# Kernel optimization log

Hardware: AMD Instinct MI355X
Metric: run time of the kernel (lower is better)

Reference implementation:

```python
import jax, jax.numpy as jnp
import numpy as np

B, S, E, H, I = 32, 257, 1024, 16, 4096
D = E // H  # head_dim = 64
EPS = 1e-5


def setup_inputs() -> dict:
    key = jax.random.key(0)
    ks = jax.random.split(key, 12)
    std = 0.02
    inp = {
        'hidden_states': jax.random.normal(ks[0], (B, S, E), jnp.float32),
        'attention_mask': jnp.zeros((B, 1, S, S), jnp.float32),
        'causal_attention_mask': jnp.zeros((B, 1, S, S), jnp.float32),
        'ln1_w': jnp.ones((E,), jnp.float32),
        'ln1_b': jnp.zeros((E,), jnp.float32),
        'q_w': jax.random.normal(ks[1], (E, E), jnp.float32) * std,
        'q_b': jnp.zeros((E,), jnp.float32),
        'k_w': jax.random.normal(ks[2], (E, E), jnp.float32) * std,
        'k_b': jnp.zeros((E,), jnp.float32),
        'v_w': jax.random.normal(ks[3], (E, E), jnp.float32) * std,
        'v_b': jnp.zeros((E,), jnp.float32),
        'o_w': jax.random.normal(ks[4], (E, E), jnp.float32) * std,
        'o_b': jnp.zeros((E,), jnp.float32),
        'ln2_w': jnp.ones((E,), jnp.float32),
        'ln2_b': jnp.zeros((E,), jnp.float32),
        'fc1_w': jax.random.normal(ks[5], (I, E), jnp.float32) * std,
        'fc1_b': jnp.zeros((I,), jnp.float32),
        'fc2_w': jax.random.normal(ks[6], (E, I), jnp.float32) * std,
        'fc2_b': jnp.zeros((E,), jnp.float32),
    }
    return inp


def _layernorm(x, w, b):
    mu = jnp.mean(x, axis=-1, keepdims=True)
    var = jnp.mean(jnp.square(x - mu), axis=-1, keepdims=True)
    return (x - mu) * jax.lax.rsqrt(var + EPS) * w + b


def _gelu_tanh(x):
    # 0.5*x*(1+tanh(sqrt(2/pi)*(x+0.044715*x^3)))
    c = np.sqrt(2.0 / np.pi).astype(np.float32)
    return 0.5 * x * (1.0 + jnp.tanh(c * (x + 0.044715 * x * x * x)))


def reference(hidden_states, attention_mask, causal_attention_mask,
              ln1_w, ln1_b, q_w, q_b, k_w, k_b, v_w, v_b, o_w, o_b,
              ln2_w, ln2_b, fc1_w, fc1_b, fc2_w, fc2_b):
    scale = D ** -0.5
    residual = hidden_states
    x = _layernorm(hidden_states, ln1_w, ln1_b)

    # projections (torch Linear: x @ W.T + b), q pre-scaled as in source
    q = (x @ q_w.T + q_b) * scale
    k = x @ k_w.T + k_b
    v = x @ v_w.T + v_b

    # [B, H, S, D]
    q = q.reshape(B, S, H, D).transpose(0, 2, 1, 3)
    k = k.reshape(B, S, H, D).transpose(0, 2, 1, 3)
    v = v.reshape(B, S, H, D).transpose(0, 2, 1, 3)

    scores = jnp.einsum('bhqd,bhkd->bhqk', q, k)  # [B,H,S,S]
    scores = scores + causal_attention_mask + attention_mask
    probs = jax.nn.softmax(scores, axis=-1)
    ctx = jnp.einsum('bhqk,bhkd->bhqd', probs, v)
    ctx = ctx.transpose(0, 2, 1, 3).reshape(B, S, E)
    attn_out = ctx @ o_w.T + o_b

    h = residual + attn_out
    residual = h
    x = _layernorm(h, ln2_w, ln2_b)
    x = _gelu_tanh(x @ fc1_w.T + fc1_b)
    x = x @ fc2_w.T + fc2_b
    return residual + x
```

## Files before the change

kernel.cpp:

```cpp
#include <hip/hip_runtime.h>

typedef unsigned short u16;
typedef unsigned int   u32;
typedef short s16x8 __attribute__((ext_vector_type(8)));
typedef float f32x4 __attribute__((ext_vector_type(4)));

#define MFMA16(A,B,C) __builtin_amdgcn_mfma_f32_16x16x32_bf16((A),(B),(C),0,0,0)
#define BAR()  asm volatile("s_barrier" ::: "memory")
#define LGKM0  asm volatile("s_waitcnt lgkmcnt(0)" ::: "memory")
#define VMC2   asm volatile("s_waitcnt vmcnt(2)" ::: "memory")
#define VMC0   asm volatile("s_waitcnt vmcnt(0)" ::: "memory")

#define B_   32
#define S_   257
#define E_   1024
#define H_   16
#define D_   64
#define I_   4096
#define M_   (B_*S_)

__device__ __forceinline__ u16 f2bf(float f) {
    u32 u = __float_as_uint(f);
    u32 r = u + 0x7fffu + ((u >> 16) & 1u);
    return (u16)(r >> 16);
}
__device__ __forceinline__ float bf2f(u16 b) {
    return __uint_as_float(((u32)b) << 16);
}

__device__ __forceinline__ void gload16(const void* g, void* l) {
    __builtin_amdgcn_global_load_lds(
        (const __attribute__((address_space(1))) u32*)g,
        (__attribute__((address_space(3))) u32*)l, 16, 0, 0);
}

__global__ __launch_bounds__(256)
void convert_w_kernel(const float* __restrict__ qw, const float* __restrict__ kw,
                      const float* __restrict__ vw, const float* __restrict__ ow,
                      const float* __restrict__ f1, const float* __restrict__ f2,
                      u16* __restrict__ dst)
{
    const int total4 = (12 * 1048576) / 4;
    for (int i = blockIdx.x * 256 + threadIdx.x; i < total4; i += gridDim.x * 256) {
        int e = i * 4;
        int seg = e >> 20;
        const float* srcp; int off;
        if (seg < 4)      { srcp = (seg == 0 ? qw : seg == 1 ? kw : seg == 2 ? vw : ow); off = e & 1048575; }
        else if (seg < 8) { srcp = f1; off = e - 4 * 1048576; }
        else              { srcp = f2; off = e - 8 * 1048576; }
        float4 v = *(const float4*)(srcp + off);
        ushort4 o;
        o.x = f2bf(v.x); o.y = f2bf(v.y); o.z = f2bf(v.z); o.w = f2bf(v.w);
        *(ushort4*)(dst + e) = o;
    }
}

__global__ __launch_bounds__(256)
void mask_combine_kernel(const float* __restrict__ am, const float* __restrict__ cm,
                         u16* __restrict__ msum)
{
    const int total = B_ * S_ * 272;
    for (int i = blockIdx.x * 256 + threadIdx.x; i < total; i += gridDim.x * 256) {
        int skv = i % 272;
        int rem = i / 272;
        int sq  = rem % S_;
        int b   = rem / S_;
        float v;
        if (skv < S_) {
            size_t o = ((size_t)b * S_ + sq) * S_ + skv;
            v = am[o] + cm[o];
        } else v = -1e30f;
        msum[i] = f2bf(v);
    }
}

__global__ __launch_bounds__(256)
void ln_kernel(const float* __restrict__ src, const float* __restrict__ gam,
               const float* __restrict__ bet, u16* __restrict__ dst)
{
    int row = blockIdx.x;
    const float4* p = (const float4*)(src + (size_t)row * E_);
    float4 x = p[threadIdx.x];
    float s  = x.x + x.y + x.z + x.w;
    float s2 = x.x * x.x + x.y * x.y + x.z * x.z + x.w * x.w;
#pragma unroll
    for (int xm = 1; xm < 64; xm <<= 1) {
        s  += __shfl_xor(s,  xm, 64);
        s2 += __shfl_xor(s2, xm, 64);
    }
    __shared__ float red[8];
    int wv = threadIdx.x >> 6;
    if ((threadIdx.x & 63) == 0) { red[wv] = s; red[4 + wv] = s2; }
    __syncthreads();
    s  = red[0] + red[1] + red[2] + red[3];
    s2 = red[4] + red[5] + red[6] + red[7];
    float mu  = s * (1.0f / 1024.0f);
    float var = s2 * (1.0f / 1024.0f) - mu * mu;
    float rs  = rsqrtf(var + 1e-5f);
    float4 g  = ((const float4*)gam)[threadIdx.x];
    float4 be = ((const float4*)bet)[threadIdx.x];
    ushort4 o;
    o.x = f2bf((x.x - mu) * rs * g.x + be.x);
    o.y = f2bf((x.y - mu) * rs * g.y + be.y);
    o.z = f2bf((x.z - mu) * rs * g.z + be.z);
    o.w = f2bf((x.w - mu) * rs * g.w + be.w);
    ((ushort4*)dst)[(size_t)row * 256 + threadIdx.x] = o;
}

template<int MODE>
__global__ __launch_bounds__(512, 2)
void gemm8(const u16* __restrict__ A,
           const u16* __restrict__ Bq, const u16* __restrict__ Bk, const u16* __restrict__ Bv,
           const float* __restrict__ biasq, const float* __restrict__ biask, const float* __restrict__ biasvv,
           const float* __restrict__ res, float* __restrict__ outF, float* __restrict__ outF1,
           u16* __restrict__ outBq, u16* __restrict__ outBk, u16* __restrict__ outBv,
           int M, int N, int Ks, int klen)
{
    __shared__ u16 lds[2][4][8192];
    const int tid = threadIdx.x, lane = tid & 63, w = tid >> 6;
    const int lr = lane & 15, lg = lane >> 4;
    const int wm = w >> 2, wn = w & 3;

    const u16* Bm = Bq; const float* bias = biasq; u16* outB = outBq;
    float scl = 1.0f; int nt = blockIdx.x; int k0 = 0; float* outP = outF;
    if (MODE == 0) {
        int mat = nt >> 2; nt &= 3;
        if (mat == 1)      { Bm = Bk; bias = biask; outB = outBk; }
        else if (mat == 2) { Bm = Bv; bias = biasvv; outB = outBv; }
        if (mat == 0) scl = 0.125f;
    } else if (MODE == 3) {
        int kz = nt & 1; nt >>= 1;
        k0 = kz * klen;
        if (kz) outP = outF1;
    }
    const int m0 = blockIdx.y * 256, n0 = nt * 256;
    const int NT = klen >> 6, NI = klen >> 7;
    const int tb = k0 >> 6;

    {
    }
    const int p    = w * 1024 + lane * 16;
    const int lby  = p ^ (((p >> 7) & 7) << 4);
    const int srow = lby >> 7;
    const int scol = (lby & 127) >> 1;

    auto STAGE = [&](int buf, int half, const u16* src, int grow0, int rowmax, int t) {
#pragma unroll
        for (int s = 0; s < 2; ++s) {
            int gr = grow0 + s * 64 + srow; if (gr > rowmax) gr = rowmax;
            gload16(src + (size_t)gr * Ks + ((tb + t) << 6) + scol,
                    (char*)&lds[buf][half][0] + s * 8192 + w * 1024);
        }
    };
    auto LDA = [&](int buf, int mh, int mf, int kh) -> s16x8 {
        const char* b = (const char*)&lds[buf][wm][0];
        int inrow = mh * 64 + mf * 16 + lr;
        return *(const s16x8*)(b + inrow * 128 + ((kh * 64 + lg * 16) ^ ((lr & 7) << 4)));
    };
    auto LDB = [&](int buf, int nh, int nf, int kh) -> s16x8 {
        const char* b = (const char*)&lds[buf][2 + (wn >> 1)][0];
        int inrow = (wn & 1) * 64 + nh * 32 + nf * 16 + lr;
        return *(const s16x8*)(b + inrow * 128 + ((kh * 64 + lg * 16) ^ ((lr & 7) << 4)));
    };

    f32x4 acc[8][4];
#pragma unroll
    for (int i = 0; i < 8; ++i)
#pragma unroll
        for (int j = 0; j < 4; ++j) { f32x4 z = {0.f, 0.f, 0.f, 0.f}; acc[i][j] = z; }

    s16x8 a[4][2], b[2][2][2];
    auto MFQ = [&](int mh, int nh) {
        __builtin_amdgcn_s_setprio(1);
#pragma unroll
        for (int mf = 0; mf < 4; ++mf)
#pragma unroll
            for (int nf = 0; nf < 2; ++nf)
#pragma unroll
                for (int kh = 0; kh < 2; ++kh)
                    acc[mh * 4 + mf][nh * 2 + nf] =
                        MFMA16(a[mf][kh], b[nh][nf][kh], acc[mh * 4 + mf][nh * 2 + nf]);
        __builtin_amdgcn_s_setprio(0);
    };

    STAGE(0, 0, A,  m0,       M - 1, 0);
    STAGE(0, 1, A,  m0 + 128, M - 1, 0);
    STAGE(0, 2, Bm, n0,       N - 1, 0);
    STAGE(0, 3, Bm, n0 + 128, N - 1, 0);
    STAGE(1, 0, A,  m0,       M - 1, 1);
    VMC2;
    BAR();

    for (int i = 0; i < NI; ++i) {
        const int t1 = 2 * i + 1, t2 = 2 * i + 2, t3 = 2 * i + 3;
        const bool more = (i + 1 < NI);
#pragma unroll
        for (int mf = 0; mf < 4; ++mf)
#pragma unroll
            for (int kh = 0; kh < 2; ++kh) a[mf][kh] = LDA(0, 0, mf, kh);
#pragma unroll
        for (int nf = 0; nf < 2; ++nf)
#pragma unroll
            for (int kh = 0; kh < 2; ++kh) b[0][nf][kh] = LDB(0, 0, nf, kh);
        STAGE(1, 1, A, m0 + 128, M - 1, t1);
        BAR(); LGKM0;
        MFQ(0, 0);
        BAR();
#pragma unroll
        for (int nf = 0; nf < 2; ++nf)
#pragma unroll
            for (int kh = 0; kh < 2; ++kh) b[1][nf][kh] = LDB(0, 1, nf, kh);
        STAGE(1, 2, Bm, n0, N - 1, t1);
        BAR(); LGKM0;
        MFQ(0, 1);
        BAR();
#pragma unroll
        for (int mf = 0; mf < 4; ++mf)
#pragma unroll
            for (int kh = 0; kh < 2; ++kh) a[mf][kh] = LDA(0, 1, mf, kh);
        STAGE(1, 3, Bm, n0 + 128, N - 1, t1);
        BAR(); LGKM0;
        MFQ(1, 1);
        BAR();
        if (more) STAGE(0, 0, A, m0, M - 1, t2);
        MFQ(1, 0);
        if (more) { VMC2; } else { VMC0; }
        BAR();
#pragma unroll
        for (int mf = 0; mf < 4; ++mf)
#pragma unroll
            for (int kh = 0; kh < 2; ++kh) a[mf][kh] = LDA(1, 0, mf, kh);
#pragma unroll
        for (int nf = 0; nf < 2; ++nf)
#pragma unroll
            for (int kh = 0; kh < 2; ++kh) b[0][nf][kh] = LDB(1, 0, nf, kh);
        if (more) STAGE(0, 2, Bm, n0, N - 1, t2);
        BAR(); LGKM0;
        MFQ(0, 0);
        BAR();
#pragma unroll
        for (int nf = 0; nf < 2; ++nf)
#pragma unroll
            for (int kh = 0; kh < 2; ++kh) b[1][nf][kh] = LDB(1, 1, nf, kh);
        if (more) STAGE(0, 3, Bm, n0 + 128, N - 1, t2);
        BAR(); LGKM0;
        MFQ(0, 1);
        BAR();
#pragma unroll
        for (int mf = 0; mf < 4; ++mf)
#pragma unroll
            for (int kh = 0; kh < 2; ++kh) a[mf][kh] = LDA(1, 1, mf, kh);
        if (more) STAGE(0, 1, A, m0 + 128, M - 1, t2);
        BAR(); LGKM0;
        MFQ(1, 1);
        BAR();
        if (more) STAGE(1, 0, A, m0, M - 1, t3);
        MFQ(1, 0);
        if (more) VMC2;
        BAR();
    }

    float biasv[4];
    if (MODE != 3) {
#pragma unroll
        for (int an = 0; an < 4; ++an)
            biasv[an] = bias[n0 + wn * 64 + (an >> 1) * 32 + (an & 1) * 16 + lr];
    }
#pragma unroll
    for (int am = 0; am < 8; ++am) {
#pragma unroll
        for (int r = 0; r < 4; ++r) {
            int row = m0 + wm * 128 + (am >> 2) * 64 + (am & 3) * 16 + lg * 4 + r;
            if (row >= M) continue;
            if (MODE == 0) {
                int bb = row / S_;
                int ss = row - bb * S_;
#pragma unroll
                for (int an = 0; an < 4; ++an) {
                    int col = n0 + wn * 64 + (an >> 1) * 32 + (an & 1) * 16 + lr;
                    int hh = col >> 6, dd = col & 63;
                    float v = (acc[am][an][r] + biasv[an]) * scl;
                    outB[(((size_t)bb * H_ + hh) * S_ + ss) * D_ + dd] = f2bf(v);
                }
            } else if (MODE == 1) {
                size_t base = (size_t)row * N;
#pragma unroll
                for (int an = 0; an < 4; ++an) {
                    int col = n0 + wn * 64 + (an >> 1) * 32 + (an & 1) * 16 + lr;
                    outF[base + col] = acc[am][an][r] + biasv[an] + res[base + col];
                }
            } else if (MODE == 2) {
                size_t base = (size_t)row * N;
#pragma unroll
                for (int an = 0; an < 4; ++an) {
                    int col = n0 + wn * 64 + (an >> 1) * 32 + (an & 1) * 16 + lr;
                    float x = acc[am][an][r] + biasv[an];
                    float u = 0.7978845608028654f * (x + 0.044715f * x * x * x);
                    float t = tanhf(u);
                    outB[base + col] = f2bf(0.5f * x * (1.0f + t));
                }
            } else {
                size_t base = (size_t)row * N;
#pragma unroll
                for (int an = 0; an < 4; ++an) {
                    int col = n0 + wn * 64 + (an >> 1) * 32 + (an & 1) * 16 + lr;
                    outP[base + col] = acc[am][an][r];
                }
            }
        }
    }
}

__global__ __launch_bounds__(256)
void fc2_reduce(const float* __restrict__ P0, const float* __restrict__ P1,
                const float* __restrict__ res, const float* __restrict__ bias,
                float* __restrict__ out)
{
    const int n4 = (M_ * E_) / 4;
    for (int i = blockIdx.x * 256 + threadIdx.x; i < n4; i += gridDim.x * 256) {
        float4 x0 = ((const float4*)P0)[i];
        float4 x1 = ((const float4*)P1)[i];
        float4 rr = ((const float4*)res)[i];
        float4 bb = ((const float4*)bias)[i & 255];
        float4 o;
        o.x = x0.x + x1.x + rr.x + bb.x;
        o.y = x0.y + x1.y + rr.y + bb.y;
        o.z = x0.z + x1.z + rr.z + bb.z;
        o.w = x0.w + x1.w + rr.w + bb.w;
        ((float4*)out)[i] = o;
    }
}

__global__ __launch_bounds__(256)
void attn_kernel(const u16* __restrict__ qg_, const u16* __restrict__ kg_,
                 const u16* __restrict__ vg_, const u16* __restrict__ msum,
                 u16* __restrict__ ctx)
{
    __shared__ u16 Ks[272 * 72];
    __shared__ u16 Vt[64 * 296];
    __shared__ u16 Ps[4][16 * 32];
    const int bh = blockIdx.x;
    const int b = bh >> 4, hh = bh & 15;
    const u16* kg = kg_ + (size_t)bh * (S_ * D_);
    const u16* vg = vg_ + (size_t)bh * (S_ * D_);
    const u16* qg = qg_ + (size_t)bh * (S_ * D_);
    const int tid = threadIdx.x, lane = tid & 63, wv = tid >> 6;

    for (int c = tid; c < (S_ * D_) / 8; c += 256) {
        int s = c >> 3, d8 = (c & 7) << 3;
        s16x8 val = *(const s16x8*)(kg + s * 64 + d8);
        *(s16x8*)&Ks[s * 72 + d8] = val;
    }
    for (int idx = tid; idx < 15 * 64; idx += 256) {
        int rr = 257 + (idx >> 6), cc = idx & 63;
        Ks[rr * 72 + cc] = 0;
    }
    for (int c = tid; c < (S_ * D_) / 8; c += 256) {
        int s = c >> 3, d8 = (c & 7) << 3;
        s16x8 val = *(const s16x8*)(vg + s * 64 + d8);
#pragma unroll
        for (int j = 0; j < 8; ++j) Vt[(d8 + j) * 296 + s] = (u16)val[j];
    }
    for (int idx = tid; idx < 64 * 39; idx += 256) {
        int dd = idx / 39, cc = 257 + idx % 39;
        Vt[dd * 296 + cc] = 0;
    }
    __syncthreads();

    const int lr = lane & 15, lg = lane >> 4;
    for (int qb = wv; qb < 17; qb += 4) {
        const int q0 = qb * 16;
        int qrow = q0 + lr; if (qrow > S_ - 1) qrow = S_ - 1;
        s16x8 aq0 = *(const s16x8*)(qg + qrow * 64 + lg * 8);
        s16x8 aq1 = *(const s16x8*)(qg + qrow * 64 + 32 + lg * 8);

        f32x4 sc[17];
#pragma unroll
        for (int t = 0; t < 17; ++t) { f32x4 z = {0.f, 0.f, 0.f, 0.f}; sc[t] = z; }
#pragma unroll
        for (int t = 0; t < 17; ++t) {
            s16x8 b0 = *(const s16x8*)&Ks[(t * 16 + lr) * 72 + lg * 8];
            s16x8 b1 = *(const s16x8*)&Ks[(t * 16 + lr) * 72 + 32 + lg * 8];
            sc[t] = MFMA16(aq0, b0, sc[t]);
            sc[t] = MFMA16(aq1, b1, sc[t]);
        }
        float mx[4] = {-3e38f, -3e38f, -3e38f, -3e38f};
#pragma unroll
        for (int r = 0; r < 4; ++r) {
            int sq = q0 + lg * 4 + r; if (sq > S_ - 1) sq = S_ - 1;
            const u16* mrow = msum + ((size_t)b * S_ + sq) * 272;
#pragma unroll
            for (int t = 0; t < 17; ++t) {
                sc[t][r] += bf2f(mrow[t * 16 + lr]);
                mx[r] = fmaxf(mx[r], sc[t][r]);
            }
        }
#pragma unroll
        for (int r = 0; r < 4; ++r) {
#pragma unroll
            for (int xm = 1; xm <= 8; xm <<= 1)
                mx[r] = fmaxf(mx[r], __shfl_xor(mx[r], xm, 64));
        }
        float sum[4] = {0.f, 0.f, 0.f, 0.f};
#pragma unroll
        for (int t = 0; t < 17; ++t)
#pragma unroll
            for (int r = 0; r < 4; ++r) {
                float e = __expf(sc[t][r] - mx[r]);
                sc[t][r] = e; sum[r] += e;
            }
#pragma unroll
        for (int r = 0; r < 4; ++r) {
#pragma unroll
            for (int xm = 1; xm <= 8; xm <<= 1)
                sum[r] += __shfl_xor(sum[r], xm, 64);
        }

        f32x4 ac[4];
#pragma unroll
        for (int nt = 0; nt < 4; ++nt) { f32x4 z = {0.f, 0.f, 0.f, 0.f}; ac[nt] = z; }
        u16* myP = &Ps[wv][0];
#pragma unroll
        for (int kc = 0; kc < 9; ++kc) {
#pragma unroll
            for (int tt = 0; tt < 2; ++tt) {
                const int t = kc * 2 + tt;
#pragma unroll
                for (int r = 0; r < 4; ++r) {
                    float pv = (t < 17) ? sc[(t < 17) ? t : 0][r] : 0.f;
                    myP[(lg * 4 + r) * 32 + tt * 16 + lr] = f2bf(pv);
                }
            }
            s16x8 pa = *(const s16x8*)&myP[lr * 32 + lg * 8];
#pragma unroll
            for (int nt = 0; nt < 4; ++nt) {
                s16x8 bv = *(const s16x8*)&Vt[(nt * 16 + lr) * 296 + kc * 32 + lg * 8];
                ac[nt] = MFMA16(pa, bv, ac[nt]);
            }
        }
#pragma unroll
        for (int r = 0; r < 4; ++r) {
            int sq = q0 + lg * 4 + r;
            if (sq < S_) {
                float rd = 1.0f / sum[r];
                size_t base = (((size_t)b * S_ + sq) * H_ + hh) * D_;
#pragma unroll
                for (int nt = 0; nt < 4; ++nt)
                    ctx[base + nt * 16 + lr] = f2bf(ac[nt][r] * rd);
            }
        }
    }
}

extern "C" void kernel_launch(void* const* d_in, const int* in_sizes, int n_in,
                              void* d_out, int out_size, void* d_ws, size_t ws_size,
                              hipStream_t stream)
{
    const float* hid   = (const float*)d_in[0];
    const float* am    = (const float*)d_in[1];
    const float* cm    = (const float*)d_in[2];
    const float* ln1w  = (const float*)d_in[3];
    const float* ln1b  = (const float*)d_in[4];
    const float* qw    = (const float*)d_in[5];
    const float* qbias = (const float*)d_in[6];
    const float* kw    = (const float*)d_in[7];
    const float* kbias = (const float*)d_in[8];
    const float* vw    = (const float*)d_in[9];
    const float* vbias = (const float*)d_in[10];
    const float* ow    = (const float*)d_in[11];
    const float* obias = (const float*)d_in[12];
    const float* ln2w  = (const float*)d_in[13];
    const float* ln2b  = (const float*)d_in[14];
    const float* f1w   = (const float*)d_in[15];
    const float* f1b   = (const float*)d_in[16];
    const float* f2w   = (const float*)d_in[17];
    const float* f2b   = (const float*)d_in[18];
    float* out = (float*)d_out;

    const size_t ME = (size_t)M_ * E_;
    u16* Wq   = (u16*)d_ws;
    u16* Wk   = Wq + 1048576;
    u16* Wv   = Wk + 1048576;
    u16* Wo   = Wv + 1048576;
    u16* Wf1  = Wo + 1048576;
    u16* Wf2  = Wf1 + 4 * 1048576;
    u16* xln  = Wf2 + 4 * 1048576;
    u16* qb_  = xln + ME;
    u16* kb_  = qb_ + ME;
    u16* vb_  = kb_ + ME;
    u16* ctx  = vb_ + ME;
    float* hbuf = (float*)(ctx + ME);
    u16* msum = (u16*)(hbuf + ME);
    u16* act  = qb_;
    u16* x2   = xln;
    float* P0 = (float*)(msum + (size_t)B_ * S_ * 272);
    float* P1 = P0 + ME;
    const size_t need = (size_t)((char*)(P1 + ME) - (char*)d_ws);
    const bool split = ws_size >= need;

    convert_w_kernel<<<3072, 256, 0, stream>>>(qw, kw, vw, ow, f1w, f2w, Wq);
    mask_combine_kernel<<<8736, 256, 0, stream>>>(am, cm, msum);
    ln_kernel<<<M_, 256, 0, stream>>>(hid, ln1w, ln1b, xln);
    gemm8<0><<<dim3(12, 33), 512, 0, stream>>>(xln, Wq, Wk, Wv, qbias, kbias, vbias,
                                               nullptr, nullptr, nullptr, qb_, kb_, vb_,
                                               M_, 1024, 1024, 1024);
    attn_kernel<<<512, 256, 0, stream>>>(qb_, kb_, vb_, msum, ctx);
    gemm8<1><<<dim3(4, 33), 512, 0, stream>>>(ctx, Wo, nullptr, nullptr, obias, nullptr, nullptr,
                                              hid, hbuf, nullptr, nullptr, nullptr, nullptr,
                                              M_, 1024, 1024, 1024);
    ln_kernel<<<M_, 256, 0, stream>>>(hbuf, ln2w, ln2b, x2);
    gemm8<2><<<dim3(16, 33), 512, 0, stream>>>(x2, Wf1, nullptr, nullptr, f1b, nullptr, nullptr,
                                               nullptr, nullptr, nullptr, act, nullptr, nullptr,
                                               M_, 4096, 1024, 1024);
    if (split) {
        gemm8<3><<<dim3(8, 33), 512, 0, stream>>>(act, Wf2, nullptr, nullptr, nullptr, nullptr, nullptr,
                                                  nullptr, P0, P1, nullptr, nullptr, nullptr,
                                                  M_, 1024, 4096, 2048);
        fc2_reduce<<<2048, 256, 0, stream>>>(P0, P1, hbuf, f2b, out);
    } else {
        gemm8<1><<<dim3(4, 33), 512, 0, stream>>>(act, Wf2, nullptr, nullptr, f2b, nullptr, nullptr,
                                                  hbuf, out, nullptr, nullptr, nullptr, nullptr,
                                                  M_, 1024, 4096, 4096);
    }
}
```

Before: 451.2 us.

## Deepen GEMM prefetch, drop FC2 split-K, use exp-based GELU

The GEMM main loop now issues all four quarter-tile loads for the next K-step at once and waits with a looser vmcnt, so more global loads are in flight before the barrier. The split-K path for FC2 (two partial outputs plus a separate reduce kernel) is removed, and FC2 runs as a single full-K GEMM with a fused residual and bias epilogue. GELU tanh is rewritten as x*sigmoid(2u) using __expf with clamping, which avoids tanhf. The FC2 grid shrinks to 132 blocks, which may leave CUs underused, and the deeper prefetch changes wait placement.

New measurement: 421.6 us. 6.6% less time.

```diff
diff --git a/kernel.cpp b/kernel.cpp
--- a/kernel.cpp
+++ b/kernel.cpp
@@ -8,7 +8,7 @@
 #define MFMA16(A,B,C) __builtin_amdgcn_mfma_f32_16x16x32_bf16((A),(B),(C),0,0,0)
 #define BAR()  asm volatile("s_barrier" ::: "memory")
 #define LGKM0  asm volatile("s_waitcnt lgkmcnt(0)" ::: "memory")
-#define VMC2   asm volatile("s_waitcnt vmcnt(2)" ::: "memory")
+#define VMC8   asm volatile("s_waitcnt vmcnt(8)" ::: "memory")
 #define VMC0   asm volatile("s_waitcnt vmcnt(0)" ::: "memory")
 
 #define B_   32
@@ -112,9 +112,9 @@
 void gemm8(const u16* __restrict__ A,
            const u16* __restrict__ Bq, const u16* __restrict__ Bk, const u16* __restrict__ Bv,
            const float* __restrict__ biasq, const float* __restrict__ biask, const float* __restrict__ biasvv,
-           const float* __restrict__ res, float* __restrict__ outF, float* __restrict__ outF1,
+           const float* __restrict__ res, float* __restrict__ outF,
            u16* __restrict__ outBq, u16* __restrict__ outBk, u16* __restrict__ outBv,
-           int M, int N, int Ks, int klen)
+           int M, int N, int K)
 {
     __shared__ u16 lds[2][4][8192];
     const int tid = threadIdx.x, lane = tid & 63, w = tid >> 6;
@@ -122,23 +122,16 @@
     const int wm = w >> 2, wn = w & 3;
 
     const u16* Bm = Bq; const float* bias = biasq; u16* outB = outBq;
-    float scl = 1.0f; int nt = blockIdx.x; int k0 = 0; float* outP = outF;
+    float scl = 1.0f; int nt = blockIdx.x;
     if (MODE == 0) {
         int mat = nt >> 2; nt &= 3;
         if (mat == 1)      { Bm = Bk; bias = biask; outB = outBk; }
         else if (mat == 2) { Bm = Bv; bias = biasvv; outB = outBv; }
         if (mat == 0) scl = 0.125f;
-    } else if (MODE == 3) {
-        int kz = nt & 1; nt >>= 1;
-        k0 = kz * klen;
-        if (kz) outP = outF1;
     }
     const int m0 = blockIdx.y * 256, n0 = nt * 256;
-    const int NT = klen >> 6, NI = klen >> 7;
-    const int tb = k0 >> 6;
-
-    {
-    }
+    const int NI = K >> 7;
+
     const int p    = w * 1024 + lane * 16;
     const int lby  = p ^ (((p >> 7) & 7) << 4);
     const int srow = lby >> 7;
@@ -148,7 +141,7 @@
 #pragma unroll
         for (int s = 0; s < 2; ++s) {
             int gr = grow0 + s * 64 + srow; if (gr > rowmax) gr = rowmax;
-            gload16(src + (size_t)gr * Ks + ((tb + t) << 6) + scol,
+            gload16(src + (size_t)gr * K + (t << 6) + scol,
                     (char*)&lds[buf][half][0] + s * 8192 + w * 1024);
         }
     };
@@ -188,11 +181,14 @@
     STAGE(0, 2, Bm, n0,       N - 1, 0);
     STAGE(0, 3, Bm, n0 + 128, N - 1, 0);
     STAGE(1, 0, A,  m0,       M - 1, 1);
-    VMC2;
+    STAGE(1, 1, A,  m0 + 128, M - 1, 1);
+    STAGE(1, 2, Bm, n0,       N - 1, 1);
+    STAGE(1, 3, Bm, n0 + 128, N - 1, 1);
+    VMC8;
     BAR();
 
     for (int i = 0; i < NI; ++i) {
-        const int t1 = 2 * i + 1, t2 = 2 * i + 2, t3 = 2 * i + 3;
+        const int t2 = 2 * i + 2, t3 = 2 * i + 3;
         const bool more = (i + 1 < NI);
 #pragma unroll
         for (int mf = 0; mf < 4; ++mf)
@@ -202,7 +198,6 @@
         for (int nf = 0; nf < 2; ++nf)
 #pragma unroll
             for (int kh = 0; kh < 2; ++kh) b[0][nf][kh] = LDB(0, 0, nf, kh);
-        STAGE(1, 1, A, m0 + 128, M - 1, t1);
         BAR(); LGKM0;
         MFQ(0, 0);
         BAR();
@@ -210,7 +205,6 @@
         for (int nf = 0; nf < 2; ++nf)
 #pragma unroll
             for (int kh = 0; kh < 2; ++kh) b[1][nf][kh] = LDB(0, 1, nf, kh);
-        STAGE(1, 2, Bm, n0, N - 1, t1);
         BAR(); LGKM0;
         MFQ(0, 1);
         BAR();
@@ -218,13 +212,19 @@
         for (int mf = 0; mf < 4; ++mf)
 #pragma unroll
             for (int kh = 0; kh < 2; ++kh) a[mf][kh] = LDA(0, 1, mf, kh);
-        STAGE(1, 3, Bm, n0 + 128, N - 1, t1);
+        if (more) {
+            STAGE(0, 2, Bm, n0,       N - 1, t2);
+            STAGE(0, 3, Bm, n0 + 128, N - 1, t2);
+        }
         BAR(); LGKM0;
         MFQ(1, 1);
         BAR();
-        if (more) STAGE(0, 0, A, m0, M - 1, t2);
+        if (more) {
+            STAGE(0, 0, A, m0,       M - 1, t2);
+            STAGE(0, 1, A, m0 + 128, M - 1, t2);
+        }
         MFQ(1, 0);
-        if (more) { VMC2; } else { VMC0; }
+        if (more) { VMC8; } else { VMC0; }
         BAR();
 #pragma unroll
         for (int mf = 0; mf < 4; ++mf)
@@ -234,7 +234,6 @@
         for (int nf = 0; nf < 2; ++nf)
 #pragma unroll
             for (int kh = 0; kh < 2; ++kh) b[0][nf][kh] = LDB(1, 0, nf, kh);
-        if (more) STAGE(0, 2, Bm, n0, N - 1, t2);
         BAR(); LGKM0;
         MFQ(0, 0);
         BAR();
@@ -242,7 +241,6 @@
         for (int nf = 0; nf < 2; ++nf)
 #pragma unroll
             for (int kh = 0; kh < 2; ++kh) b[1][nf][kh] = LDB(1, 1, nf, kh);
-        if (more) STAGE(0, 3, Bm, n0 + 128, N - 1, t2);
         BAR(); LGKM0;
         MFQ(0, 1);
         BAR();
@@ -250,22 +248,29 @@
         for (int mf = 0; mf < 4; ++mf)
 #pragma unroll
             for (int kh = 0; kh < 2; ++kh) a[mf][kh] = LDA(1, 1, mf, kh);
-        if (more) STAGE(0, 1, A, m0 + 128, M - 1, t2);
+        if (more) {
+            STAGE(1, 2, Bm, n0,       N - 1, t3);
+            STAGE(1, 3, Bm, n0 + 128, N - 1, t3);
+        }
         BAR(); LGKM0;
         MFQ(1, 1);
         BAR();
-        if (more) STAGE(1, 0, A, m0, M - 1, t3);
-        MFQ(1, 0);
-        if (more) VMC2;
+        if (more) {
+            STAGE(1, 0, A, m0,       M - 1, t3);
+            STAGE(1, 1, A, m0 + 128, M - 1, t3);
+            MFQ(1, 0);
+            VMC8;
+        } else {
+            MFQ(1, 0);
+        }
         BAR();
     }
 
     float biasv[4];
-    if (MODE != 3) {
-#pragma unroll
-        for (int an = 0; an < 4; ++an)
-            biasv[an] = bias[n0 + wn * 64 + (an >> 1) * 32 + (an & 1) * 16 + lr];
-    }
+#pragma unroll
+    for (int an = 0; an < 4; ++an)
+        biasv[an] = bias[n0 + wn * 64 + (an >> 1) * 32 + (an & 1) * 16 + lr];
+
 #pragma unroll
     for (int am = 0; am < 8; ++am) {
 #pragma unroll
@@ -289,45 +294,19 @@
                     int col = n0 + wn * 64 + (an >> 1) * 32 + (an & 1) * 16 + lr;
                     outF[base + col] = acc[am][an][r] + biasv[an] + res[base + col];
                 }
-            } else if (MODE == 2) {
+            } else {
                 size_t base = (size_t)row * N;
 #pragma unroll
                 for (int an = 0; an < 4; ++an) {
                     int col = n0 + wn * 64 + (an >> 1) * 32 + (an & 1) * 16 + lr;
                     float x = acc[am][an][r] + biasv[an];
-                    float u = 0.7978845608028654f * (x + 0.044715f * x * x * x);
-                    float t = tanhf(u);
-                    outB[base + col] = f2bf(0.5f * x * (1.0f + t));
+                    float u2 = 1.5957691216057308f * (x + 0.044715f * x * x * x);
+                    u2 = fminf(u2, 80.0f);
+                    float t = __expf(u2);
+                    outB[base + col] = f2bf(x * t / (1.0f + t));
                 }
-            } else {
-                size_t base = (size_t)row * N;
-#pragma unroll
-                for (int an = 0; an < 4; ++an) {
-                    int col = n0 + wn * 64 + (an >> 1) * 32 + (an & 1) * 16 + lr;
-                    outP[base + col] = acc[am][an][r];
-                }
-            }
-        }
-    }
-}
-
-__global__ __launch_bounds__(256)
-void fc2_reduce(const float* __restrict__ P0, const float* __restrict__ P1,
-                const float* __restrict__ res, const float* __restrict__ bias,
-                float* __restrict__ out)
-{
-    const int n4 = (M_ * E_) / 4;
-    for (int i = blockIdx.x * 256 + threadIdx.x; i < n4; i += gridDim.x * 256) {
-        float4 x0 = ((const float4*)P0)[i];
-        float4 x1 = ((const float4*)P1)[i];
-        float4 rr = ((const float4*)res)[i];
-        float4 bb = ((const float4*)bias)[i & 255];
-        float4 o;
-        o.x = x0.x + x1.x + rr.x + bb.x;
-        o.y = x0.y + x1.y + rr.y + bb.y;
-        o.z = x0.z + x1.z + rr.z + bb.z;
-        o.w = x0.w + x1.w + rr.w + bb.w;
-        ((float4*)out)[i] = o;
+            }
+        }
     }
 }
 
@@ -493,33 +472,22 @@
     u16* msum = (u16*)(hbuf + ME);
     u16* act  = qb_;
     u16* x2   = xln;
-    float* P0 = (float*)(msum + (size_t)B_ * S_ * 272);
-    float* P1 = P0 + ME;
-    const size_t need = (size_t)((char*)(P1 + ME) - (char*)d_ws);
-    const bool split = ws_size >= need;
 
     convert_w_kernel<<<3072, 256, 0, stream>>>(qw, kw, vw, ow, f1w, f2w, Wq);
     mask_combine_kernel<<<8736, 256, 0, stream>>>(am, cm, msum);
     ln_kernel<<<M_, 256, 0, stream>>>(hid, ln1w, ln1b, xln);
     gemm8<0><<<dim3(12, 33), 512, 0, stream>>>(xln, Wq, Wk, Wv, qbias, kbias, vbias,
-                                               nullptr, nullptr, nullptr, qb_, kb_, vb_,
-                                               M_, 1024, 1024, 1024);
+                                               nullptr, nullptr, qb_, kb_, vb_,
+                                               M_, 1024, 1024);
     attn_kernel<<<512, 256, 0, stream>>>(qb_, kb_, vb_, msum, ctx);
     gemm8<1><<<dim3(4, 33), 512, 0, stream>>>(ctx, Wo, nullptr, nullptr, obias, nullptr, nullptr,
-                                              hid, hbuf, nullptr, nullptr, nullptr, nullptr,
-                                              M_, 1024, 1024, 1024);
+                                              hid, hbuf, nullptr, nullptr, nullptr,
+                                              M_, 1024, 1024);
     ln_kernel<<<M_, 256, 0, stream>>>(hbuf, ln2w, ln2b, x2);
     gemm8<2><<<dim3(16, 33), 512, 0, stream>>>(x2, Wf1, nullptr, nullptr, f1b, nullptr, nullptr,
-                                               nullptr, nullptr, nullptr, act, nullptr, nullptr,
-                                               M_, 4096, 1024, 1024);
-    if (split) {
-        gemm8<3><<<dim3(8, 33), 512, 0, stream>>>(act, Wf2, nullptr, nullptr, nullptr, nullptr, nullptr,
-                                                  nullptr, P0, P1, nullptr, nullptr, nullptr,
-                                                  M_, 1024, 4096, 2048);
-        fc2_reduce<<<2048, 256, 0, stream>>>(P0, P1, hbuf, f2b, out);
-    } else {
-        gemm8<1><<<dim3(4, 33), 512, 0, stream>>>(act, Wf2, nullptr, nullptr, f2b, nullptr, nullptr,
-                                                  hbuf, out, nullptr, nullptr, nullptr, nullptr,
-                                                  M_, 1024, 4096, 4096);
-    }
-}
+                                               nullptr, nullptr, act, nullptr, nullptr,
+                                               M_, 4096, 1024);
+    gemm8<1><<<dim3(4, 33), 512, 0, stream>>>(act, Wf2, nullptr, nullptr, f2b, nullptr, nullptr,
+                                              hbuf, out, nullptr, nullptr, nullptr,
+                                              M_, 1024, 4096);
+}
```
